# Optimization experiments

Hardware: AMD Instinct MI355X
Metric: run time of the kernel (lower is better)

The kernel has to match this reference:

```python
import jax, jax.numpy as jnp
import numpy as np

N_NODES = 100000
HIDDEN = 128
N_EDGES = 1000000


def setup_inputs() -> dict:
    key = jax.random.key(0)
    k1, k2, k3 = jax.random.split(key, 3)
    z = jax.random.normal(k1, (N_NODES, HIDDEN), dtype=jnp.float32)
    edge_index = jax.random.randint(k2, (2, N_EDGES), 0, N_NODES, dtype=jnp.int64)
    # xavier_uniform for square matrix: bound = sqrt(6/(fan_in+fan_out))
    bound = float(np.sqrt(6.0 / (HIDDEN + HIDDEN)))
    weights = jax.random.uniform(k3, (HIDDEN, HIDDEN), dtype=jnp.float32,
                                 minval=-bound, maxval=bound)
    return {"z": z, "edge_index": edge_index, "weights": weights}


def reference(z, edge_index, weights):
    # symm=True: symmetrize the bilinear form
    W = weights + weights.T                      # [d, d]
    z_src = z[edge_index[0]]                     # [E, d] gather
    z_dst = z[edge_index[1]]                     # [E, d] gather
    # torch: (W @ z_dst.T).T == z_dst @ W.T
    value = jnp.einsum('ed,dk,ek->e', z_src, W, z_dst)  # row-wise bilinear score
    return jax.nn.sigmoid(value)
```

## Files before the change

kernel.cpp:

```cpp
#include <hip/hip_runtime.h>

#define HIDDEN 128
#define LDSW 136
#define BSHIFT 10
#define NBMAX 128
#define CAP 10752
#define OVF_MAX 65536

typedef _Float16 f16;
typedef f16 f16x2 __attribute__((ext_vector_type(2)));
typedef f16 f16x8 __attribute__((ext_vector_type(8)));
typedef float f32x16 __attribute__((ext_vector_type(16)));
typedef unsigned long long ull;
typedef ull ull2 __attribute__((ext_vector_type(2)));

static __device__ __forceinline__ float fdot2(f16x2 a, f16x2 b, float c) {
    return __builtin_amdgcn_fdot2(a, b, c, false);
}

__global__ __launch_bounds__(256) void prep_w(const float* __restrict__ w,
                                              f16* __restrict__ wsh_t,
                                              int* __restrict__ cursor,
                                              int* __restrict__ ovf_cnt) {
    int idx = blockIdx.x * 256 + threadIdx.x;
    if (idx < NBMAX) cursor[idx] = idx * CAP;
    if (idx == NBMAX) ovf_cnt[0] = 0;
    int n = idx >> 7, k = idx & 127;
    wsh_t[idx] = (f16)(w[k * HIDDEN + n] + w[n * HIDDEN + k]);
}

__global__ __launch_bounds__(256) void gemm_scatter(const float* __restrict__ z,
                                                    const f16* __restrict__ wsh_t,
                                                    f16* __restrict__ zh,
                                                    f16* __restrict__ uh,
                                                    const int* __restrict__ eidx,
                                                    int* __restrict__ cursor,
                                                    ull* __restrict__ perm,
                                                    ull* __restrict__ ovf,
                                                    int* __restrict__ ovf_cnt,
                                                    int nrows, int E, int nb, int ngemm) {
    __shared__ f16 wlt[HIDDEN * LDSW];
    int tid = threadIdx.x;

    if (blockIdx.x >= ngemm) {
        int* lh    = (int*)wlt;
        int* lbase = lh + NBMAX;
        int* lrank = lbase + NBMAX;
        int base = (blockIdx.x - ngemm) * 4096;
        if (tid < NBMAX) { lh[tid] = 0; lrank[tid] = 0; }
        __syncthreads();
        int s[16], d[16], bb[16];
        #pragma unroll
        for (int i = 0; i < 16; ++i) {
            int e = base + i * 256 + tid;
            bb[i] = -1;
            if (e < E) {
                s[i] = eidx[e]; d[i] = eidx[E + e];
                bb[i] = d[i] >> BSHIFT;
                atomicAdd(&lh[bb[i]], 1);
            }
        }
        __syncthreads();
        if (tid < nb && lh[tid]) lbase[tid] = atomicAdd(&cursor[tid], lh[tid]);
        __syncthreads();
        #pragma unroll
        for (int i = 0; i < 16; ++i) {
            if (bb[i] >= 0) {
                int e = base + i * 256 + tid;
                int r = atomicAdd(&lrank[bb[i]], 1);
                long pos = (long)lbase[bb[i]] + r;
                ull v = (ull)s[i] | ((ull)d[i] << 17) | ((ull)(e + 1) << 34);
                if (pos < (long)(bb[i] + 1) * CAP) perm[pos] = v;
                else {
                    int o = atomicAdd(ovf_cnt, 1);
                    if (o < OVF_MAX) ovf[o] = v;
                }
            }
        }
        return;
    }

    {
        const f16x8* g = (const f16x8*)wsh_t;
        #pragma unroll
        for (int it = 0; it < 8; ++it) {
            int idx = it * 256 + tid;
            int j = idx >> 4, kc = idx & 15;
            *(f16x8*)&wlt[j * LDSW + kc * 8] = g[idx];
        }
    }
    __syncthreads();

    int wave = tid >> 6, lane = tid & 63;
    int row0 = blockIdx.x * 128 + wave * 32;
    if (row0 > nrows - 32) row0 = nrows - 32;

    int m = lane & 31, half = lane >> 5;
    const float* zr = z  + (size_t)(row0 + m) * HIDDEN + half * 8;
    f16*        zhr = zh + (size_t)(row0 + m) * HIDDEN + half * 8;
    const f16* wbase = &wlt[m * LDSW + half * 8];

    f32x16 acc0, acc1, acc2, acc3;
    #pragma unroll
    for (int r = 0; r < 16; ++r) { acc0[r] = 0.f; acc1[r] = 0.f; acc2[r] = 0.f; acc3[r] = 0.f; }

    #pragma unroll
    for (int ks = 0; ks < 8; ++ks) {
        float4 a0 = *(const float4*)(zr + 16 * ks);
        float4 a1 = *(const float4*)(zr + 16 * ks + 4);
        f16x8 af = {(f16)a0.x, (f16)a0.y, (f16)a0.z, (f16)a0.w,
                    (f16)a1.x, (f16)a1.y, (f16)a1.z, (f16)a1.w};
        *(f16x8*)(zhr + 16 * ks) = af;
        f16x8 b0 = *(const f16x8*)(wbase + 16 * ks);
        f16x8 b1 = *(const f16x8*)(wbase + 32 * LDSW + 16 * ks);
        f16x8 b2 = *(const f16x8*)(wbase + 64 * LDSW + 16 * ks);
        f16x8 b3 = *(const f16x8*)(wbase + 96 * LDSW + 16 * ks);
        acc0 = __builtin_amdgcn_mfma_f32_32x32x16_f16(af, b0, acc0, 0, 0, 0);
        acc1 = __builtin_amdgcn_mfma_f32_32x32x16_f16(af, b1, acc1, 0, 0, 0);
        acc2 = __builtin_amdgcn_mfma_f32_32x32x16_f16(af, b2, acc2, 0, 0, 0);
        acc3 = __builtin_amdgcn_mfma_f32_32x32x16_f16(af, b3, acc3, 0, 0, 0);
    }

    f16* ur = uh + (size_t)row0 * HIDDEN;
    #pragma unroll
    for (int r = 0; r < 16; ++r) {
        int row = (r & 3) + 8 * (r >> 2) + 4 * half;
        f16* p = ur + (size_t)row * HIDDEN + m;
        p[0]  = (f16)acc0[r];
        p[32] = (f16)acc1[r];
        p[64] = (f16)acc2[r];
        p[96] = (f16)acc3[r];
    }
}

static __device__ __forceinline__ void score_edge(const f16* uh, const f16* zh,
                                                  ull p, float* out, int t, int E) {
    int src = (int)(p & 0x1FFFF);
    int dst = (int)((p >> 17) & 0x1FFFF);
    int ep  = (int)(p >> 34);
    const float4* a4 = (const float4*)(uh + (size_t)src * HIDDEN);
    const float4* b4 = (const float4*)(zh + (size_t)dst * HIDDEN);
    float4 av = a4[t], bv = b4[t];
    const f16x2* ap = (const f16x2*)&av;
    const f16x2* bp = (const f16x2*)&bv;
    float s = 0.f;
    #pragma unroll
    for (int i = 0; i < 4; ++i) s = fdot2(ap[i], bp[i], s);
    #pragma unroll
    for (int off = 8; off > 0; off >>= 1) s += __shfl_down(s, off, 16);
    if (t == 0 && ep > 0 && ep <= E) out[ep - 1] = 1.0f / (1.0f + __expf(-s));
}

__global__ __launch_bounds__(256, 8) void edge_bin(const f16* __restrict__ uh,
                                                   const f16* __restrict__ zh,
                                                   const ull* __restrict__ perm,
                                                   const ull* __restrict__ ovf,
                                                   const int* __restrict__ ovf_cnt,
                                                   float* __restrict__ out,
                                                   int E, int cpx, int nmain) {
    int tid = threadIdx.x;
    int g = tid >> 4, t = tid & 15;
    int blk = blockIdx.x;
    if (blk >= nmain) {
        int n = ovf_cnt[0];
        if (n > OVF_MAX) n = OVF_MAX;
        for (int i = (blk - nmain) * 16 + g; i < n; i += 32 * 16)
            score_edge(uh, zh, ovf[i], out, t, E);
        return;
    }
    int chunk = (blk & 7) * cpx + (blk >> 3);
    long slot = (long)chunk * 64 + g * 4;
    ull2 pa = *(const ull2*)&perm[slot];
    ull2 pb = *(const ull2*)&perm[slot + 2];

    int src0 = (int)(pa.x & 0x1FFFF), dst0 = (int)((pa.x >> 17) & 0x1FFFF), e0 = (int)(pa.x >> 34);
    int src1 = (int)(pa.y & 0x1FFFF), dst1 = (int)((pa.y >> 17) & 0x1FFFF), e1 = (int)(pa.y >> 34);
    int src2 = (int)(pb.x & 0x1FFFF), dst2 = (int)((pb.x >> 17) & 0x1FFFF), e2 = (int)(pb.x >> 34);
    int src3 = (int)(pb.y & 0x1FFFF), dst3 = (int)((pb.y >> 17) & 0x1FFFF), e3 = (int)(pb.y >> 34);

    float4 va0 = ((const float4*)(uh + (size_t)src0 * HIDDEN))[t];
    float4 vb0 = ((const float4*)(zh + (size_t)dst0 * HIDDEN))[t];
    float4 va1 = ((const float4*)(uh + (size_t)src1 * HIDDEN))[t];
    float4 vb1 = ((const float4*)(zh + (size_t)dst1 * HIDDEN))[t];
    float4 va2 = ((const float4*)(uh + (size_t)src2 * HIDDEN))[t];
    float4 vb2 = ((const float4*)(zh + (size_t)dst2 * HIDDEN))[t];
    float4 va3 = ((const float4*)(uh + (size_t)src3 * HIDDEN))[t];
    float4 vb3 = ((const float4*)(zh + (size_t)dst3 * HIDDEN))[t];

    const f16x2* ap0 = (const f16x2*)&va0; const f16x2* bp0 = (const f16x2*)&vb0;
    const f16x2* ap1 = (const f16x2*)&va1; const f16x2* bp1 = (const f16x2*)&vb1;
    const f16x2* ap2 = (const f16x2*)&va2; const f16x2* bp2 = (const f16x2*)&vb2;
    const f16x2* ap3 = (const f16x2*)&va3; const f16x2* bp3 = (const f16x2*)&vb3;
    float s0 = 0.f, s1 = 0.f, s2 = 0.f, s3 = 0.f;
    #pragma unroll
    for (int i = 0; i < 4; ++i) {
        s0 = fdot2(ap0[i], bp0[i], s0);
        s1 = fdot2(ap1[i], bp1[i], s1);
        s2 = fdot2(ap2[i], bp2[i], s2);
        s3 = fdot2(ap3[i], bp3[i], s3);
    }
    #pragma unroll
    for (int off = 8; off > 0; off >>= 1) {
        s0 += __shfl_xor(s0, off, 16);
        s1 += __shfl_xor(s1, off, 16);
        s2 += __shfl_xor(s2, off, 16);
        s3 += __shfl_xor(s3, off, 16);
    }
    float sv = (t == 0) ? s0 : (t == 1) ? s1 : (t == 2) ? s2 : s3;
    int   ev = (t == 0) ? e0 : (t == 1) ? e1 : (t == 2) ? e2 : e3;
    if (t < 4 && ev > 0 && ev <= E) out[ev - 1] = 1.0f / (1.0f + __expf(-sv));
}

__global__ __launch_bounds__(256) void edge_score16(const f16* __restrict__ uh,
                                                    const f16* __restrict__ zh,
                                                    const int* __restrict__ eidx,
                                                    float* __restrict__ out, int E) {
    int tid = threadIdx.x;
    int g = tid >> 4, t = tid & 15;
    int e = blockIdx.x * 16 + g;
    if (e >= E) return;
    ull p = (ull)eidx[e] | ((ull)eidx[E + e] << 17) | ((ull)(e + 1) << 34);
    score_edge(uh, zh, p, out, t, E);
}

extern "C" void kernel_launch(void* const* d_in, const int* in_sizes, int n_in,
                              void* d_out, int out_size, void* d_ws, size_t ws_size,
                              hipStream_t stream) {
    const float* z    = (const float*)d_in[0];
    const int*   eidx = (const int*)d_in[1];
    const float* w    = (const float*)d_in[2];
    float* out = (float*)d_out;

    int nrows = in_sizes[0] / HIDDEN;
    int E = out_size;
    int nb = (nrows >> BSHIFT) + 1;

    f16* wsh_t  = (f16*)d_ws;
    f16* zh     = wsh_t + HIDDEN * HIDDEN;
    f16* uh     = zh + (size_t)nrows * HIDDEN;
    int* cursor = (int*)(uh + (size_t)nrows * HIDDEN);
    int* ovf_cnt = cursor + NBMAX;
    ull* ovf    = (ull*)(ovf_cnt + 4);
    ull* perm   = ovf + OVF_MAX;

    long nslots = (long)nb * CAP;
    size_t need = (size_t)((char*)(perm + nslots) - (char*)d_ws);
    bool binned = ws_size >= need;

    int ngemm = (nrows + 127) / 128;
    int nscat = (E + 4095) / 4096;

    prep_w<<<64, 256, 0, stream>>>(w, wsh_t, cursor, ovf_cnt);
    if (binned) {
        gemm_scatter<<<ngemm + nscat, 256, 0, stream>>>(z, wsh_t, zh, uh, eidx, cursor,
                                                        perm, ovf, ovf_cnt, nrows, E, nb, ngemm);
        long ngrp = nslots / 64;
        int cpx = (int)(ngrp / 8);
        int nmain = (int)ngrp;
        edge_bin<<<nmain + 32, 256, 0, stream>>>(uh, zh, perm, ovf, ovf_cnt, out, E, cpx, nmain);
    } else {
        gemm_scatter<<<ngemm, 256, 0, stream>>>(z, wsh_t, zh, uh, eidx, cursor,
                                                perm, ovf, ovf_cnt, nrows, E, nb, ngemm);
        edge_score16<<<(E + 15) / 16, 256, 0, stream>>>(uh, zh, eidx, out, E);
    }
}
```

Baseline: 159.5 us.

## Fuse GEMM, scatter and edge scoring into one persistent kernel with grid barrier

```diff
diff --git a/kernel.cpp b/kernel.cpp
--- a/kernel.cpp
+++ b/kernel.cpp
@@ -1,11 +1,11 @@
 #include <hip/hip_runtime.h>
 
 #define HIDDEN 128
-#define LDSW 136
 #define BSHIFT 10
 #define NBMAX 128
 #define CAP 10752
 #define OVF_MAX 65536
+#define SCAT_T 17
 
 typedef _Float16 f16;
 typedef f16 f16x2 __attribute__((ext_vector_type(2)));
@@ -24,81 +24,82 @@
                                               int* __restrict__ ovf_cnt) {
     int idx = blockIdx.x * 256 + threadIdx.x;
     if (idx < NBMAX) cursor[idx] = idx * CAP;
-    if (idx == NBMAX) ovf_cnt[0] = 0;
+    if (idx == NBMAX) { ovf_cnt[0] = 0; ovf_cnt[1] = 0; }
     int n = idx >> 7, k = idx & 127;
     wsh_t[idx] = (f16)(w[k * HIDDEN + n] + w[n * HIDDEN + k]);
 }
 
-__global__ __launch_bounds__(256) void gemm_scatter(const float* __restrict__ z,
-                                                    const f16* __restrict__ wsh_t,
-                                                    f16* __restrict__ zh,
-                                                    f16* __restrict__ uh,
-                                                    const int* __restrict__ eidx,
-                                                    int* __restrict__ cursor,
-                                                    ull* __restrict__ perm,
-                                                    ull* __restrict__ ovf,
-                                                    int* __restrict__ ovf_cnt,
-                                                    int nrows, int E, int nb, int ngemm) {
-    __shared__ f16 wlt[HIDDEN * LDSW];
+
+static __device__ __forceinline__ void do_scatter(f16* wlt, int sblk,
+                                                  const int* __restrict__ eidx,
+                                                  int* __restrict__ cursor,
+                                                  ull* __restrict__ perm,
+                                                  ull* __restrict__ ovf,
+                                                  int* __restrict__ ovf_cnt,
+                                                  int E, int nb) {
     int tid = threadIdx.x;
-
-    if (blockIdx.x >= ngemm) {
-        int* lh    = (int*)wlt;
-        int* lbase = lh + NBMAX;
-        int* lrank = lbase + NBMAX;
-        int base = (blockIdx.x - ngemm) * 4096;
-        if (tid < NBMAX) { lh[tid] = 0; lrank[tid] = 0; }
-        __syncthreads();
-        int s[16], d[16], bb[16];
-        #pragma unroll
-        for (int i = 0; i < 16; ++i) {
+    int* lh    = (int*)wlt;
+    int* lbase = lh + NBMAX;
+    int* lrank = lbase + NBMAX;
+    int base = sblk * (256 * SCAT_T);
+    if (tid < NBMAX) { lh[tid] = 0; lrank[tid] = 0; }
+    __syncthreads();
+    int s[SCAT_T], d[SCAT_T], bb[SCAT_T];
+    #pragma unroll
+    for (int i = 0; i < SCAT_T; ++i) {
+        int e = base + i * 256 + tid;
+        bb[i] = -1;
+        if (e < E) {
+            s[i] = eidx[e]; d[i] = eidx[E + e];
+            bb[i] = d[i] >> BSHIFT;
+            atomicAdd(&lh[bb[i]], 1);
+        }
+    }
+    __syncthreads();
+    if (tid < nb && lh[tid]) lbase[tid] = atomicAdd(&cursor[tid], lh[tid]);
+    __syncthreads();
+    #pragma unroll
+    for (int i = 0; i < SCAT_T; ++i) {
+        if (bb[i] >= 0) {
             int e = base + i * 256 + tid;
-            bb[i] = -1;
-            if (e < E) {
-                s[i] = eidx[e]; d[i] = eidx[E + e];
-                bb[i] = d[i] >> BSHIFT;
-                atomicAdd(&lh[bb[i]], 1);
+            int r = atomicAdd(&lrank[bb[i]], 1);
+            long pos = (long)lbase[bb[i]] + r;
+            ull v = (ull)s[i] | ((ull)d[i] << 17) | ((ull)(e + 1) << 34);
+            if (pos < (long)(bb[i] + 1) * CAP) perm[pos] = v;
+            else {
+                int o = atomicAdd(ovf_cnt, 1);
+                if (o < OVF_MAX) ovf[o] = v;
             }
         }
-        __syncthreads();
-        if (tid < nb && lh[tid]) lbase[tid] = atomicAdd(&cursor[tid], lh[tid]);
-        __syncthreads();
-        #pragma unroll
-        for (int i = 0; i < 16; ++i) {
-            if (bb[i] >= 0) {
-                int e = base + i * 256 + tid;
-                int r = atomicAdd(&lrank[bb[i]], 1);
-                long pos = (long)lbase[bb[i]] + r;
-                ull v = (ull)s[i] | ((ull)d[i] << 17) | ((ull)(e + 1) << 34);
-                if (pos < (long)(bb[i] + 1) * CAP) perm[pos] = v;
-                else {
-                    int o = atomicAdd(ovf_cnt, 1);
-                    if (o < OVF_MAX) ovf[o] = v;
-                }
-            }
-        }
-        return;
-    }
-
+    }
+}
+
+static __device__ __forceinline__ void do_gemm(f16* wlt, int tile,
+                                               const float* __restrict__ z,
+                                               const f16* __restrict__ wsh_t,
+                                               f16* __restrict__ zh,
+                                               f16* __restrict__ uh, int nrows) {
+    int tid = threadIdx.x;
     {
         const f16x8* g = (const f16x8*)wsh_t;
         #pragma unroll
         for (int it = 0; it < 8; ++it) {
             int idx = it * 256 + tid;
             int j = idx >> 4, kc = idx & 15;
-            *(f16x8*)&wlt[j * LDSW + kc * 8] = g[idx];
+            *(f16x8*)&wlt[j * HIDDEN + (((kc + (j & 7)) & 15) << 3)] = g[idx];
         }
     }
     __syncthreads();
 
     int wave = tid >> 6, lane = tid & 63;
-    int row0 = blockIdx.x * 128 + wave * 32;
+    int row0 = tile * 128 + wave * 32;
     if (row0 > nrows - 32) row0 = nrows - 32;
 
     int m = lane & 31, half = lane >> 5;
+    int rot = m & 7;
     const float* zr = z  + (size_t)(row0 + m) * HIDDEN + half * 8;
     f16*        zhr = zh + (size_t)(row0 + m) * HIDDEN + half * 8;
-    const f16* wbase = &wlt[m * LDSW + half * 8];
+    const f16* wrow = &wlt[m * HIDDEN];
 
     f32x16 acc0, acc1, acc2, acc3;
     #pragma unroll
@@ -111,10 +112,11 @@
         f16x8 af = {(f16)a0.x, (f16)a0.y, (f16)a0.z, (f16)a0.w,
                     (f16)a1.x, (f16)a1.y, (f16)a1.z, (f16)a1.w};
         *(f16x8*)(zhr + 16 * ks) = af;
-        f16x8 b0 = *(const f16x8*)(wbase + 16 * ks);
-        f16x8 b1 = *(const f16x8*)(wbase + 32 * LDSW + 16 * ks);
-        f16x8 b2 = *(const f16x8*)(wbase + 64 * LDSW + 16 * ks);
-        f16x8 b3 = *(const f16x8*)(wbase + 96 * LDSW + 16 * ks);
+        int c = ((half + 2 * ks + rot) & 15) << 3;
+        f16x8 b0 = *(const f16x8*)&wrow[c];
+        f16x8 b1 = *(const f16x8*)&wrow[32 * HIDDEN + c];
+        f16x8 b2 = *(const f16x8*)&wrow[64 * HIDDEN + c];
+        f16x8 b3 = *(const f16x8*)&wrow[96 * HIDDEN + c];
         acc0 = __builtin_amdgcn_mfma_f32_32x32x16_f16(af, b0, acc0, 0, 0, 0);
         acc1 = __builtin_amdgcn_mfma_f32_32x32x16_f16(af, b1, acc1, 0, 0, 0);
         acc2 = __builtin_amdgcn_mfma_f32_32x32x16_f16(af, b2, acc2, 0, 0, 0);
@@ -151,64 +153,99 @@
     if (t == 0 && ep > 0 && ep <= E) out[ep - 1] = 1.0f / (1.0f + __expf(-s));
 }
 
-__global__ __launch_bounds__(256, 8) void edge_bin(const f16* __restrict__ uh,
-                                                   const f16* __restrict__ zh,
-                                                   const ull* __restrict__ perm,
-                                                   const ull* __restrict__ ovf,
-                                                   const int* __restrict__ ovf_cnt,
-                                                   float* __restrict__ out,
-                                                   int E, int cpx, int nmain) {
+__global__ __launch_bounds__(256, 4) void fused_all(const float* __restrict__ z,
+                                                    const f16* __restrict__ wsh_t,
+                                                    f16* __restrict__ zh,
+                                                    f16* __restrict__ uh,
+                                                    const int* __restrict__ eidx,
+                                                    int* __restrict__ cursor,
+                                                    ull* __restrict__ perm,
+                                                    ull* __restrict__ ovf,
+                                                    int* __restrict__ ovf_cnt,
+                                                    float* __restrict__ out,
+                                                    int nrows, int E, int nb,
+                                                    int ngemm, int nscat, int nblk, int cpx) {
+    __shared__ f16 wlt[HIDDEN * HIDDEN];
     int tid = threadIdx.x;
+
+    if (blockIdx.x < (unsigned)ngemm)
+        do_gemm(wlt, blockIdx.x, z, wsh_t, zh, uh, nrows);
+    else if (blockIdx.x < (unsigned)(ngemm + nscat))
+        do_scatter(wlt, blockIdx.x - ngemm, eidx, cursor, perm, ovf, ovf_cnt, E, nb);
+
+    __syncthreads();
+    int* bar = ovf_cnt + 1;
+    if (tid == 0) {
+        __threadfence();
+        __hip_atomic_fetch_add(bar, 1, __ATOMIC_ACQ_REL, __HIP_MEMORY_SCOPE_AGENT);
+        int guard = 0;
+        while (__hip_atomic_load(bar, __ATOMIC_ACQUIRE, __HIP_MEMORY_SCOPE_AGENT) < nblk &&
+               ++guard < (1 << 22))
+            __builtin_amdgcn_s_sleep(8);
+    }
+    __syncthreads();
+    __threadfence();
+
     int g = tid >> 4, t = tid & 15;
-    int blk = blockIdx.x;
-    if (blk >= nmain) {
+    int x = blockIdx.x & 7, ib = blockIdx.x >> 3;
+    int nbx = (nblk - x + 7) >> 3;
+    for (int c = ib; c < cpx; c += nbx) {
+        long slot = ((long)x * cpx + c) * 64 + g * 4;
+        ull2 pa = *(const ull2*)&perm[slot];
+        ull2 pb = *(const ull2*)&perm[slot + 2];
+
+        int src0 = (int)(pa.x & 0x1FFFF), dst0 = (int)((pa.x >> 17) & 0x1FFFF), e0 = (int)(pa.x >> 34);
+        int src1 = (int)(pa.y & 0x1FFFF), dst1 = (int)((pa.y >> 17) & 0x1FFFF), e1 = (int)(pa.y >> 34);
+        int src2 = (int)(pb.x & 0x1FFFF), dst2 = (int)((pb.x >> 17) & 0x1FFFF), e2 = (int)(pb.x >> 34);
+        int src3 = (int)(pb.y & 0x1FFFF), dst3 = (int)((pb.y >> 17) & 0x1FFFF), e3 = (int)(pb.y >> 34);
+
+        float4 va0 = ((const float4*)(uh + (size_t)src0 * HIDDEN))[t];
+        float4 vb0 = ((const float4*)(zh + (size_t)dst0 * HIDDEN))[t];
+        float4 va1 = ((const float4*)(uh + (size_t)src1 * HIDDEN))[t];
+        float4 vb1 = ((const float4*)(zh + (size_t)dst1 * HIDDEN))[t];
+        float4 va2 = ((const float4*)(uh + (size_t)src2 * HIDDEN))[t];
+        float4 vb2 = ((const float4*)(zh + (size_t)dst2 * HIDDEN))[t];
+        float4 va3 = ((const float4*)(uh + (size_t)src3 * HIDDEN))[t];
+        float4 vb3 = ((const float4*)(zh + (size_t)dst3 * HIDDEN))[t];
+
+        const f16x2* ap0 = (const f16x2*)&va0; const f16x2* bp0 = (const f16x2*)&vb0;
+        const f16x2* ap1 = (const f16x2*)&va1; const f16x2* bp1 = (const f16x2*)&vb1;
+        const f16x2* ap2 = (const f16x2*)&va2; const f16x2* bp2 = (const f16x2*)&vb2;
+        const f16x2* ap3 = (const f16x2*)&va3; const f16x2* bp3 = (const f16x2*)&vb3;
+        float s0 = 0.f, s1 = 0.f, s2 = 0.f, s3 = 0.f;
+        #pragma unroll
+        for (int i = 0; i < 4; ++i) {
+            s0 = fdot2(ap0[i], bp0[i], s0);
+            s1 = fdot2(ap1[i], bp1[i], s1);
+            s2 = fdot2(ap2[i], bp2[i], s2);
+            s3 = fdot2(ap3[i], bp3[i], s3);
+        }
+        #pragma unroll
+        for (int off = 8; off > 0; off >>= 1) {
+            s0 += __shfl_xor(s0, off, 16);
+            s1 += __shfl_xor(s1, off, 16);
+            s2 += __shfl_xor(s2, off, 16);
+            s3 += __shfl_xor(s3, off, 16);
+        }
+        float sv = (t == 0) ? s0 : (t == 1) ? s1 : (t == 2) ? s2 : s3;
+        int   ev = (t == 0) ? e0 : (t == 1) ? e1 : (t == 2) ? e2 : e3;
+        if (t < 4 && ev > 0 && ev <= E) out[ev - 1] = 1.0f / (1.0f + __expf(-sv));
+    }
+
+    if (blockIdx.x < 32) {
         int n = ovf_cnt[0];
         if (n > OVF_MAX) n = OVF_MAX;
-        for (int i = (blk - nmain) * 16 + g; i < n; i += 32 * 16)
+        for (int i = blockIdx.x * 16 + g; i < n; i += 32 * 16)
             score_edge(uh, zh, ovf[i], out, t, E);
-        return;
-    }
-    int chunk = (blk & 7) * cpx + (blk >> 3);
-    long slot = (long)chunk * 64 + g * 4;
-    ull2 pa = *(const ull2*)&perm[slot];
-    ull2 pb = *(const ull2*)&perm[slot + 2];
-
-    int src0 = (int)(pa.x & 0x1FFFF), dst0 = (int)((pa.x >> 17) & 0x1FFFF), e0 = (int)(pa.x >> 34);
-    int src1 = (int)(pa.y & 0x1FFFF), dst1 = (int)((pa.y >> 17) & 0x1FFFF), e1 = (int)(pa.y >> 34);
-    int src2 = (int)(pb.x & 0x1FFFF), dst2 = (int)((pb.x >> 17) & 0x1FFFF), e2 = (int)(pb.x >> 34);
-    int src3 = (int)(pb.y & 0x1FFFF), dst3 = (int)((pb.y >> 17) & 0x1FFFF), e3 = (int)(pb.y >> 34);
-
-    float4 va0 = ((const float4*)(uh + (size_t)src0 * HIDDEN))[t];
-    float4 vb0 = ((const float4*)(zh + (size_t)dst0 * HIDDEN))[t];
-    float4 va1 = ((const float4*)(uh + (size_t)src1 * HIDDEN))[t];
-    float4 vb1 = ((const float4*)(zh + (size_t)dst1 * HIDDEN))[t];
-    float4 va2 = ((const float4*)(uh + (size_t)src2 * HIDDEN))[t];
-    float4 vb2 = ((const float4*)(zh + (size_t)dst2 * HIDDEN))[t];
-    float4 va3 = ((const float4*)(uh + (size_t)src3 * HIDDEN))[t];
-    float4 vb3 = ((const float4*)(zh + (size_t)dst3 * HIDDEN))[t];
-
-    const f16x2* ap0 = (const f16x2*)&va0; const f16x2* bp0 = (const f16x2*)&vb0;
-    const f16x2* ap1 = (const f16x2*)&va1; const f16x2* bp1 = (const f16x2*)&vb1;
-    const f16x2* ap2 = (const f16x2*)&va2; const f16x2* bp2 = (const f16x2*)&vb2;
-    const f16x2* ap3 = (const f16x2*)&va3; const f16x2* bp3 = (const f16x2*)&vb3;
-    float s0 = 0.f, s1 = 0.f, s2 = 0.f, s3 = 0.f;
-    #pragma unroll
-    for (int i = 0; i < 4; ++i) {
-        s0 = fdot2(ap0[i], bp0[i], s0);
-        s1 = fdot2(ap1[i], bp1[i], s1);
-        s2 = fdot2(ap2[i], bp2[i], s2);
-        s3 = fdot2(ap3[i], bp3[i], s3);
-    }
-    #pragma unroll
-    for (int off = 8; off > 0; off >>= 1) {
-        s0 += __shfl_xor(s0, off, 16);
-        s1 += __shfl_xor(s1, off, 16);
-        s2 += __shfl_xor(s2, off, 16);
-        s3 += __shfl_xor(s3, off, 16);
-    }
-    float sv = (t == 0) ? s0 : (t == 1) ? s1 : (t == 2) ? s2 : s3;
-    int   ev = (t == 0) ? e0 : (t == 1) ? e1 : (t == 2) ? e2 : e3;
-    if (t < 4 && ev > 0 && ev <= E) out[ev - 1] = 1.0f / (1.0f + __expf(-sv));
+    }
+}
+
+__global__ __launch_bounds__(256) void gemm_only(const float* __restrict__ z,
+                                                 const f16* __restrict__ wsh_t,
+                                                 f16* __restrict__ zh,
+                                                 f16* __restrict__ uh, int nrows) {
+    __shared__ f16 wlt[HIDDEN * HIDDEN];
+    do_gemm(wlt, blockIdx.x, z, wsh_t, zh, uh, nrows);
 }
 
 __global__ __launch_bounds__(256) void edge_score16(const f16* __restrict__ uh,
@@ -248,19 +285,17 @@
     bool binned = ws_size >= need;
 
     int ngemm = (nrows + 127) / 128;
-    int nscat = (E + 4095) / 4096;
+    int nscat = (E + 256 * SCAT_T - 1) / (256 * SCAT_T);
 
     prep_w<<<64, 256, 0, stream>>>(w, wsh_t, cursor, ovf_cnt);
     if (binned) {
-        gemm_scatter<<<ngemm + nscat, 256, 0, stream>>>(z, wsh_t, zh, uh, eidx, cursor,
-                                                        perm, ovf, ovf_cnt, nrows, E, nb, ngemm);
-        long ngrp = nslots / 64;
-        int cpx = (int)(ngrp / 8);
-        int nmain = (int)ngrp;
-        edge_bin<<<nmain + 32, 256, 0, stream>>>(uh, zh, perm, ovf, ovf_cnt, out, E, cpx, nmain);
+        int nblk = 1024;
+        int cpx = (int)(nslots / 64 / 8);
+        fused_all<<<nblk, 256, 0, stream>>>(z, wsh_t, zh, uh, eidx, cursor,
+                                            perm, ovf, ovf_cnt, out,
+                                            nrows, E, nb, ngemm, nscat, nblk, cpx);
     } else {
-        gemm_scatter<<<ngemm, 256, 0, stream>>>(z, wsh_t, zh, uh, eidx, cursor,
-                                                perm, ovf, ovf_cnt, nrows, E, nb, ngemm);
+        gemm_only<<<ngemm, 256, 0, stream>>>(z, wsh_t, zh, uh, nrows);
         edge_score16<<<(E + 15) / 16, 256, 0, stream>>>(uh, zh, eidx, out, E);
     }
 }
```

Result: slower. 468.8 us (+194.0%).
